# Optimization experiments

Hardware: AMD Instinct MI355X
Metric: run time of the kernel (lower is better)

## Reference

```python
import jax, jax.numpy as jnp
import numpy as np

EMBED_DIM = 1024

def setup_inputs() -> dict:
    key = jax.random.key(0)
    ks = jax.random.split(key, 7)
    D = EMBED_DIM
    x = jax.random.normal(ks[0], (4, 2048, D), dtype=jnp.float32)
    s = 1.0 / np.sqrt(D)
    Wq = jax.random.normal(ks[1], (D, D), dtype=jnp.float32) * s
    bq = jnp.zeros((D,), dtype=jnp.float32)
    Wk = jax.random.normal(ks[2], (D, D), dtype=jnp.float32) * s
    bk = jnp.zeros((D,), dtype=jnp.float32)
    Wv = jax.random.normal(ks[3], (D, D), dtype=jnp.float32) * s
    bv = jnp.zeros((D,), dtype=jnp.float32)
    return {"x": x, "Wq": Wq, "bq": bq, "Wk": Wk, "bk": bk, "Wv": Wv, "bv": bv}

def reference(x, Wq, bq, Wk, bk, Wv, bv):
    # x: [B,S,D]; torch Linear: x @ W.T + b -> here W is stored as [D_in, D_out]
    Q = jnp.einsum('bsd,de->bse', x, Wq) + bq
    K = jnp.einsum('bsd,de->bse', x, Wk) + bk
    V = jnp.einsum('bsd,de->bse', x, Wv) + bv
    scale = 1.0 / jnp.sqrt(jnp.asarray(x.shape[-1], dtype=x.dtype))
    scores = jnp.einsum('bqd,bkd->bqk', Q, K) * scale  # [B,S,S]
    probs = jax.nn.softmax(scores, axis=-1)
    # dropout is identity in eval mode
    return jnp.einsum('bqk,bkd->bqd', probs, V)
```

## Files before the change

### kernel.cpp

```cpp
#include <hip/hip_runtime.h>
#include <hip/hip_bf16.h>
#include <hip/hip_fp16.h>
#include <stdint.h>
#include <stddef.h>
#include <string.h>

#define D_EMB 1024
#define SEQ   2048
#define BATCH 4

typedef short bf16x8  __attribute__((ext_vector_type(8)));
typedef short short8  __attribute__((ext_vector_type(8)));
typedef float f32x4   __attribute__((ext_vector_type(4)));

#define AS1 __attribute__((address_space(1)))
#define AS3 __attribute__((address_space(3)))

static __device__ __forceinline__ void async_copy16(const void* g, void* l) {
  __builtin_amdgcn_global_load_lds((const AS1 void*)g, (AS3 void*)l, 16, 0, 0);
}

static __device__ __forceinline__ void gemm128(
    const __hip_bfloat16* __restrict__ A, int lda,
    const __hip_bfloat16* __restrict__ Bt, int ldb,
    int K, f32x4 (&acc)[4][4])
{
  __shared__ __hip_bfloat16 ldsA[2][128 * 64];
  __shared__ __hip_bfloat16 ldsB[2][128 * 64];

  const int t    = threadIdx.x;
  const int wave = t >> 6;
  const int lane = t & 63;
  const int quad = lane >> 4;
  const int lr   = lane & 15;
  const int wr   = wave >> 1;
  const int wc   = wave & 1;

  const int r0 = t >> 3;
  const int c0 = (((t & 7) ^ (r0 & 7)) * 8);

  const __hip_bfloat16* gA = A  + (size_t)r0 * lda + c0;
  const __hip_bfloat16* gB = Bt + (size_t)r0 * ldb + c0;

  const int niter = K >> 6;

  {
    char* lA = (char*)ldsA[0] + wave * 1024;
    char* lB = (char*)ldsB[0] + wave * 1024;
#pragma unroll
    for (int ch = 0; ch < 4; ch++) {
      async_copy16(gA + (size_t)(32 * ch) * lda, lA + 4096 * ch);
      async_copy16(gB + (size_t)(32 * ch) * ldb, lB + 4096 * ch);
    }
  }

  int buf = 0;
  for (int it = 0; it < niter; ++it) {
    __syncthreads();

    if (it + 1 < niter) {
      const int k0 = (it + 1) << 6;
      char* lA = (char*)ldsA[buf ^ 1] + wave * 1024;
      char* lB = (char*)ldsB[buf ^ 1] + wave * 1024;
#pragma unroll
      for (int ch = 0; ch < 4; ch++) {
        async_copy16(gA + k0 + (size_t)(32 * ch) * lda, lA + 4096 * ch);
        async_copy16(gB + k0 + (size_t)(32 * ch) * ldb, lB + 4096 * ch);
      }
    }

    const __hip_bfloat16* bA = ldsA[buf];
    const __hip_bfloat16* bB = ldsB[buf];
#pragma unroll
    for (int kk = 0; kk < 64; kk += 32) {
      bf16x8 aF[4], bF[4];
      const int lc = (kk >> 3) + quad;
      const int pc = (lc ^ (lr & 7)) * 8;
#pragma unroll
      for (int i = 0; i < 4; i++)
        aF[i] = *(const bf16x8*)&bA[(wr * 64 + i * 16 + lr) * 64 + pc];
#pragma unroll
      for (int j = 0; j < 4; j++)
        bF[j] = *(const bf16x8*)&bB[(wc * 64 + j * 16 + lr) * 64 + pc];

#pragma unroll
      for (int i = 0; i < 4; i++)
#pragma unroll
        for (int j = 0; j < 4; j++)
          acc[i][j] = __builtin_amdgcn_mfma_f32_16x16x32_bf16(aF[i], bF[j], acc[i][j], 0, 0, 0);
    }
    buf ^= 1;
  }
}

#define ZERO_ACC(acc)                         \
  {                                           \
    f32x4 _z = {0.f, 0.f, 0.f, 0.f};          \
    _Pragma("unroll")                         \
    for (int _i = 0; _i < 4; _i++)            \
      _Pragma("unroll")                       \
      for (int _j = 0; _j < 4; _j++)          \
        acc[_i][_j] = _z;                     \
  }

__global__ __launch_bounds__(256) void prep_kernel(
    const float* __restrict__ x,
    const float* __restrict__ Wq,
    const float* __restrict__ Wk,
    const float* __restrict__ Wv,
    __hip_bfloat16* __restrict__ xb,
    __hip_bfloat16* __restrict__ Wt3)
{
  const int tx = threadIdx.x, ty = threadIdx.y;
  if (blockIdx.z == 3) {
    const int tid = ty * 32 + tx;
    const size_t base = ((size_t)blockIdx.y * 32 + blockIdx.x) * 8192;
#pragma unroll
    for (int p = 0; p < 8; p++) {
      const size_t i = base + p * 1024 + tid * 4;
      const float4 v = *(const float4*)(x + i);
      __hip_bfloat16 o[4] = {__float2bfloat16(v.x), __float2bfloat16(v.y),
                             __float2bfloat16(v.z), __float2bfloat16(v.w)};
      *(uint64_t*)(xb + i) = *(uint64_t*)o;
    }
    return;
  }
  const float* src = (blockIdx.z == 0) ? Wq : (blockIdx.z == 1) ? Wk : Wv;
  __hip_bfloat16* dst = Wt3 + (size_t)blockIdx.z * D_EMB * D_EMB;
  __shared__ __hip_bfloat16 tile[32][33];
  const int x0 = blockIdx.x * 32;
  const int y0 = blockIdx.y * 32;
#pragma unroll
  for (int i = 0; i < 32; i += 8)
    tile[ty + i][tx] = __float2bfloat16(src[(size_t)(y0 + ty + i) * D_EMB + (x0 + tx)]);
  __syncthreads();
#pragma unroll
  for (int i = 0; i < 32; i += 8)
    dst[(size_t)(x0 + ty + i) * D_EMB + (y0 + tx)] = tile[tx][ty + i];
}

__global__ __launch_bounds__(256) void qkv_kernel(
    const __hip_bfloat16* __restrict__ xb,
    const __hip_bfloat16* __restrict__ Wt3,
    const float* __restrict__ bq,
    const float* __restrict__ bk,
    const float* __restrict__ bv,
    __hip_bfloat16* __restrict__ Q,
    __hip_bfloat16* __restrict__ Kb,
    __hip_bfloat16* __restrict__ Vt)
{
  const int mat = blockIdx.z;
  const int m0  = blockIdx.x * 128;
  const int n0  = blockIdx.y * 128;

  f32x4 acc[4][4];
  ZERO_ACC(acc);

  gemm128(xb + (size_t)m0 * D_EMB, D_EMB,
          Wt3 + (size_t)mat * D_EMB * D_EMB + (size_t)n0 * D_EMB, D_EMB,
          D_EMB, acc);

  const float* bias = (mat == 0) ? bq : (mat == 1) ? bk : bv;

  const int t = threadIdx.x;
  const int wave = t >> 6, lane = t & 63;
  const int quad = lane >> 4, lr = lane & 15;
  const int wr = wave >> 1, wc = wave & 1;

#pragma unroll
  for (int i = 0; i < 4; i++) {
#pragma unroll
    for (int j = 0; j < 4; j++) {
      const int n = n0 + wc * 64 + j * 16 + lr;
      const float bb = bias[n];
      const int mbase = m0 + wr * 64 + i * 16 + quad * 4;
      if (mat == 2) {
        const int b = mbase >> 11, s = mbase & 2047;
        __hip_bfloat16 pk[4];
#pragma unroll
        for (int r = 0; r < 4; r++) pk[r] = __float2bfloat16(acc[i][j][r] + bb);
        *(uint64_t*)&Vt[(size_t)b * D_EMB * SEQ + (size_t)n * SEQ + s] = *(uint64_t*)pk;
      } else {
        __hip_bfloat16* dst = (mat == 0) ? Q : Kb;
#pragma unroll
        for (int r = 0; r < 4; r++)
          dst[(size_t)(mbase + r) * D_EMB + n] = __float2bfloat16(acc[i][j][r] + bb);
      }
    }
  }
}

__global__ __launch_bounds__(256) void scores_kernel(
    const __hip_bfloat16* __restrict__ Q,
    const __hip_bfloat16* __restrict__ Kb,
    __half* __restrict__ Sc)
{
  const int b  = blockIdx.z;
  const int m0 = blockIdx.y * 128;
  const int n0 = blockIdx.x * 128;

  f32x4 acc[4][4];
  ZERO_ACC(acc);

  gemm128(Q  + (size_t)b * SEQ * D_EMB + (size_t)m0 * D_EMB, D_EMB,
          Kb + (size_t)b * SEQ * D_EMB + (size_t)n0 * D_EMB, D_EMB,
          D_EMB, acc);

  __half* out = Sc + (size_t)b * SEQ * SEQ;
  const float scale = 0.03125f;

  const int t = threadIdx.x;
  const int wave = t >> 6, lane = t & 63;
  const int quad = lane >> 4, lr = lane & 15;
  const int wr = wave >> 1, wc = wave & 1;

#pragma unroll
  for (int i = 0; i < 4; i++)
#pragma unroll
    for (int j = 0; j < 4; j++) {
      const int n = n0 + wc * 64 + j * 16 + lr;
#pragma unroll
      for (int r = 0; r < 4; r++) {
        const int m = m0 + wr * 64 + i * 16 + quad * 4 + r;
        out[(size_t)m * SEQ + n] = __float2half(acc[i][j][r] * scale);
      }
    }
}

__global__ __launch_bounds__(256) void softmax_kernel(
    const __half* __restrict__ Sc, __hip_bfloat16* __restrict__ P)
{
  const int row = blockIdx.x;
  const __half* src = Sc + (size_t)row * SEQ;
  const int t = threadIdx.x;
  const int wave = t >> 6, lane = t & 63;

  const short8 raw = *(const short8*)(src + t * 8);
  float v[8];
#pragma unroll
  for (int i = 0; i < 8; i++) {
    const short si = raw[i];
    __half h;
    memcpy(&h, &si, sizeof(h));
    v[i] = __half2float(h);
  }

  float m = v[0];
#pragma unroll
  for (int i = 1; i < 8; i++) m = fmaxf(m, v[i]);
#pragma unroll
  for (int o = 32; o > 0; o >>= 1) m = fmaxf(m, __shfl_xor(m, o));

  __shared__ float redm[4];
  __shared__ float reds[4];
  if (lane == 0) redm[wave] = m;
  __syncthreads();
  m = fmaxf(fmaxf(redm[0], redm[1]), fmaxf(redm[2], redm[3]));

  float e[8], s = 0.f;
#pragma unroll
  for (int i = 0; i < 8; i++) { e[i] = __expf(v[i] - m); s += e[i]; }
#pragma unroll
  for (int o = 32; o > 0; o >>= 1) s += __shfl_xor(s, o);
  if (lane == 0) reds[wave] = s;
  __syncthreads();
  s = reds[0] + reds[1] + reds[2] + reds[3];

  const float inv = 1.f / s;
  short8 outp;
#pragma unroll
  for (int i = 0; i < 8; i++) {
    const __hip_bfloat16 b = __float2bfloat16(e[i] * inv);
    short sb;
    memcpy(&sb, &b, sizeof(sb));
    outp[i] = sb;
  }
  *(short8*)(P + (size_t)row * SEQ + t * 8) = outp;
}

__global__ __launch_bounds__(256) void pv_kernel(
    const __hip_bfloat16* __restrict__ P,
    const __hip_bfloat16* __restrict__ Vt,
    float* __restrict__ out)
{
  const int b  = blockIdx.z;
  const int m0 = blockIdx.y * 128;
  const int n0 = blockIdx.x * 128;

  f32x4 acc[4][4];
  ZERO_ACC(acc);

  gemm128(P  + (size_t)b * SEQ * SEQ   + (size_t)m0 * SEQ, SEQ,
          Vt + (size_t)b * D_EMB * SEQ + (size_t)n0 * SEQ, SEQ,
          SEQ, acc);

  float* o = out + (size_t)b * SEQ * D_EMB;

  const int t = threadIdx.x;
  const int wave = t >> 6, lane = t & 63;
  const int quad = lane >> 4, lr = lane & 15;
  const int wr = wave >> 1, wc = wave & 1;

#pragma unroll
  for (int i = 0; i < 4; i++)
#pragma unroll
    for (int j = 0; j < 4; j++) {
      const int n = n0 + wc * 64 + j * 16 + lr;
#pragma unroll
      for (int r = 0; r < 4; r++) {
        const int m = m0 + wr * 64 + i * 16 + quad * 4 + r;
        o[(size_t)m * D_EMB + n] = acc[i][j][r];
      }
    }
}

extern "C" void kernel_launch(void* const* d_in, const int* in_sizes, int n_in,
                              void* d_out, int out_size, void* d_ws, size_t ws_size,
                              hipStream_t stream) {
  const float* x  = (const float*)d_in[0];
  const float* Wq = (const float*)d_in[1];
  const float* bq = (const float*)d_in[2];
  const float* Wk = (const float*)d_in[3];
  const float* bk = (const float*)d_in[4];
  const float* Wv = (const float*)d_in[5];
  const float* bv = (const float*)d_in[6];
  float* out = (float*)d_out;

  char* ws = (char*)d_ws;
  __hip_bfloat16* xb  = (__hip_bfloat16*)(ws);
  __hip_bfloat16* Wt3 = (__hip_bfloat16*)(ws + 16777216);
  __hip_bfloat16* Q   = (__hip_bfloat16*)(ws + 23068672);
  __hip_bfloat16* Kb  = (__hip_bfloat16*)(ws + 39845888);
  __hip_bfloat16* Vt  = (__hip_bfloat16*)(ws + 56623104);
  __half*         Sc  = (__half*)        (ws + 73400320);
  __hip_bfloat16* P   = (__hip_bfloat16*)(ws + 140509184);

  prep_kernel  <<<dim3(32, 32, 4), dim3(32, 8), 0, stream>>>(x, Wq, Wk, Wv, xb, Wt3);
  qkv_kernel   <<<dim3(64, 8, 3),  256,        0, stream>>>(xb, Wt3, bq, bk, bv, Q, Kb, Vt);
  scores_kernel<<<dim3(16, 16, 4), 256,        0, stream>>>(Q, Kb, Sc);
  softmax_kernel<<<dim3(8192),     256,        0, stream>>>(Sc, P);
  pv_kernel    <<<dim3(8, 16, 4),  256,        0, stream>>>(P, Vt, out);
}
```

Measured before the change: 265.4 us.

## Replace 128x128 GEMM tile with 256x256 8-wave ping-pong pipelined GEMM

Replaces the shared 128x128 double-buffered GEMM with a 256x256 tile computed by 512 threads (8 waves). Global-to-LDS staging is interleaved in half-tile chunks with MFMA quarters, using explicit vmcnt waits, barriers and s_setprio to overlap loads with compute. The larger tile raises operand reuse and cuts global traffic, and all three GEMM kernels (qkv, scores, pv) switch to the new grid and launch sizes. The cost is double the LDS and accumulator registers per block plus many barriers, and far fewer blocks, for example 128 for pv and 256 for scores on a 256-CU part, which may leave the GPU underfilled.

```diff
diff --git a/kernel.cpp b/kernel.cpp
--- a/kernel.cpp
+++ b/kernel.cpp
@@ -20,76 +20,162 @@
   __builtin_amdgcn_global_load_lds((const AS1 void*)g, (AS3 void*)l, 16, 0, 0);
 }
 
-static __device__ __forceinline__ void gemm128(
+
+#define BAR     __builtin_amdgcn_s_barrier()
+#define VMCNT4  asm volatile("s_waitcnt vmcnt(4)" ::: "memory")
+#define VMCNT0  asm volatile("s_waitcnt vmcnt(0)" ::: "memory")
+
+#define STAGE_A(buf, h, kt) do {                                              \
+    const __hip_bfloat16* _g = gA + (size_t)((h) * 128) * lda + ((kt) << 6);  \
+    char* _l = (char*)sA + (buf) * 32768 + (h) * 16384 + wave * 1024;         \
+    async_copy16(_g, _l);                                                     \
+    async_copy16(_g + (size_t)64 * lda, _l + 8192);                           \
+  } while (0)
+#define STAGE_B(buf, h, kt) do {                                              \
+    const __hip_bfloat16* _g = gB + (size_t)((h) * 128) * ldb + ((kt) << 6);  \
+    char* _l = (char*)sB + (buf) * 32768 + (h) * 16384 + wave * 1024;         \
+    async_copy16(_g, _l);                                                     \
+    async_copy16(_g + (size_t)64 * ldb, _l + 8192);                           \
+  } while (0)
+
+#define LOAD_A(aF, lbuf, h) do {                                              \
+    const __hip_bfloat16* _b = (lbuf) + (wr * 128 + (h) * 64 + lr) * 64;      \
+    _Pragma("unroll")                                                         \
+    for (int _i = 0; _i < 4; _i++) {                                          \
+      aF[_i][0] = *(const bf16x8*)&_b[_i * 1024 + pc0];                       \
+      aF[_i][1] = *(const bf16x8*)&_b[_i * 1024 + pc1];                       \
+    }                                                                         \
+  } while (0)
+#define LOAD_B(bF, lbuf, g) do {                                              \
+    const __hip_bfloat16* _b = (lbuf) + (wc * 64 + (g) * 32 + lr) * 64;       \
+    _Pragma("unroll")                                                         \
+    for (int _j = 0; _j < 2; _j++) {                                          \
+      bF[_j][0] = *(const bf16x8*)&_b[_j * 1024 + pc0];                       \
+      bF[_j][1] = *(const bf16x8*)&_b[_j * 1024 + pc1];                       \
+    }                                                                         \
+  } while (0)
+
+#define MFMA_Q(aF, bF, h, g) do {                                             \
+    __builtin_amdgcn_s_setprio(1);                                            \
+    _Pragma("unroll")                                                         \
+    for (int _i = 0; _i < 4; _i++)                                            \
+      _Pragma("unroll")                                                       \
+      for (int _j = 0; _j < 2; _j++) {                                        \
+        acc[(h) * 4 + _i][(g) * 2 + _j] =                                     \
+          __builtin_amdgcn_mfma_f32_16x16x32_bf16(aF[_i][0], bF[_j][0],       \
+              acc[(h) * 4 + _i][(g) * 2 + _j], 0, 0, 0);                      \
+        acc[(h) * 4 + _i][(g) * 2 + _j] =                                     \
+          __builtin_amdgcn_mfma_f32_16x16x32_bf16(aF[_i][1], bF[_j][1],       \
+              acc[(h) * 4 + _i][(g) * 2 + _j], 0, 0, 0);                      \
+      }                                                                       \
+    __builtin_amdgcn_s_setprio(0);                                            \
+  } while (0)
+
+static __device__ __forceinline__ void gemm256(
     const __hip_bfloat16* __restrict__ A, int lda,
     const __hip_bfloat16* __restrict__ Bt, int ldb,
-    int K, f32x4 (&acc)[4][4])
-{
-  __shared__ __hip_bfloat16 ldsA[2][128 * 64];
-  __shared__ __hip_bfloat16 ldsB[2][128 * 64];
+    int K, f32x4 (&acc)[8][4])
+{
+  __shared__ __hip_bfloat16 sA[2][128 * 64 * 2];
+  __shared__ __hip_bfloat16 sB[2][128 * 64 * 2];
 
   const int t    = threadIdx.x;
   const int wave = t >> 6;
   const int lane = t & 63;
   const int quad = lane >> 4;
   const int lr   = lane & 15;
-  const int wr   = wave >> 1;
-  const int wc   = wave & 1;
+  const int wr   = wave >> 2;
+  const int wc   = wave & 3;
 
   const int r0 = t >> 3;
-  const int c0 = (((t & 7) ^ (r0 & 7)) * 8);
-
-  const __hip_bfloat16* gA = A  + (size_t)r0 * lda + c0;
-  const __hip_bfloat16* gB = Bt + (size_t)r0 * ldb + c0;
-
-  const int niter = K >> 6;
+  const int cs = (((t & 7) ^ (r0 & 7)) << 3);
+  const __hip_bfloat16* gA = A  + (size_t)r0 * lda + cs;
+  const __hip_bfloat16* gB = Bt + (size_t)r0 * ldb + cs;
+
+  const int pc0 = ((quad)     ^ (lr & 7)) << 3;
+  const int pc1 = ((quad + 4) ^ (lr & 7)) << 3;
+
+  const __hip_bfloat16* const lA0 = sA[0];
+  const __hip_bfloat16* const lA1 = sA[1];
+  const __hip_bfloat16* const lB0 = sB[0];
+  const __hip_bfloat16* const lB1 = sB[1];
+
+  const int nt    = K >> 6;
+  const int niter = nt >> 1;
+
+  STAGE_A(0, 0, 0);
+  STAGE_A(0, 1, 0);
+  STAGE_B(0, 0, 0);
+  STAGE_B(0, 1, 0);
+  STAGE_A(1, 0, 1);
+  STAGE_B(1, 1, 1);
+  VMCNT4;
+  BAR;
+
+  bf16x8 aF[4][2], bFa[2][2], bFb[2][2];
+
+  for (int j = 0; j < niter - 1; ++j) {
+    const int tb = 2 * j + 1, tc = tb + 1, td = tb + 2;
+
+    LOAD_A(aF, lA0, 0); LOAD_B(bFa, lB0, 0);
+    STAGE_B(1, 0, tb);
+    BAR; MFMA_Q(aF, bFa, 0, 0); BAR;
+
+    LOAD_B(bFb, lB0, 1);
+    STAGE_A(1, 1, tb);
+    BAR; MFMA_Q(aF, bFb, 0, 1); BAR;
+
+    LOAD_A(aF, lA0, 1);
+    STAGE_A(0, 0, tc);
+    BAR; MFMA_Q(aF, bFb, 1, 1); BAR;
+
+    STAGE_B(0, 1, tc);
+    VMCNT4;
+    BAR; MFMA_Q(aF, bFa, 1, 0); BAR;
+
+    LOAD_A(aF, lA1, 0); LOAD_B(bFa, lB1, 0);
+    STAGE_B(0, 0, tc);
+    BAR; MFMA_Q(aF, bFa, 0, 0); BAR;
+
+    LOAD_B(bFb, lB1, 1);
+    STAGE_A(0, 1, tc);
+    BAR; MFMA_Q(aF, bFb, 0, 1); BAR;
+
+    LOAD_A(aF, lA1, 1);
+    STAGE_A(1, 0, td);
+    BAR; MFMA_Q(aF, bFb, 1, 1); BAR;
+
+    STAGE_B(1, 1, td);
+    VMCNT4;
+    BAR; MFMA_Q(aF, bFa, 1, 0); BAR;
+  }
 
   {
-    char* lA = (char*)ldsA[0] + wave * 1024;
-    char* lB = (char*)ldsB[0] + wave * 1024;
-#pragma unroll
-    for (int ch = 0; ch < 4; ch++) {
-      async_copy16(gA + (size_t)(32 * ch) * lda, lA + 4096 * ch);
-      async_copy16(gB + (size_t)(32 * ch) * ldb, lB + 4096 * ch);
-    }
-  }
-
-  int buf = 0;
-  for (int it = 0; it < niter; ++it) {
-    __syncthreads();
-
-    if (it + 1 < niter) {
-      const int k0 = (it + 1) << 6;
-      char* lA = (char*)ldsA[buf ^ 1] + wave * 1024;
-      char* lB = (char*)ldsB[buf ^ 1] + wave * 1024;
-#pragma unroll
-      for (int ch = 0; ch < 4; ch++) {
-        async_copy16(gA + k0 + (size_t)(32 * ch) * lda, lA + 4096 * ch);
-        async_copy16(gB + k0 + (size_t)(32 * ch) * ldb, lB + 4096 * ch);
-      }
-    }
-
-    const __hip_bfloat16* bA = ldsA[buf];
-    const __hip_bfloat16* bB = ldsB[buf];
-#pragma unroll
-    for (int kk = 0; kk < 64; kk += 32) {
-      bf16x8 aF[4], bF[4];
-      const int lc = (kk >> 3) + quad;
-      const int pc = (lc ^ (lr & 7)) * 8;
-#pragma unroll
-      for (int i = 0; i < 4; i++)
-        aF[i] = *(const bf16x8*)&bA[(wr * 64 + i * 16 + lr) * 64 + pc];
-#pragma unroll
-      for (int j = 0; j < 4; j++)
-        bF[j] = *(const bf16x8*)&bB[(wc * 64 + j * 16 + lr) * 64 + pc];
-
-#pragma unroll
-      for (int i = 0; i < 4; i++)
-#pragma unroll
-        for (int j = 0; j < 4; j++)
-          acc[i][j] = __builtin_amdgcn_mfma_f32_16x16x32_bf16(aF[i], bF[j], acc[i][j], 0, 0, 0);
-    }
-    buf ^= 1;
+    const int tb = nt - 1;
+    LOAD_A(aF, lA0, 0); LOAD_B(bFa, lB0, 0);
+    STAGE_B(1, 0, tb);
+    BAR; MFMA_Q(aF, bFa, 0, 0); BAR;
+
+    LOAD_B(bFb, lB0, 1);
+    STAGE_A(1, 1, tb);
+    BAR; MFMA_Q(aF, bFb, 0, 1); BAR;
+
+    LOAD_A(aF, lA0, 1);
+    BAR; MFMA_Q(aF, bFb, 1, 1); BAR;
+
+    VMCNT0;
+    BAR; MFMA_Q(aF, bFa, 1, 0); BAR;
+
+    LOAD_A(aF, lA1, 0); LOAD_B(bFa, lB1, 0);
+    BAR; MFMA_Q(aF, bFa, 0, 0); BAR;
+
+    LOAD_B(bFb, lB1, 1);
+    BAR; MFMA_Q(aF, bFb, 0, 1); BAR;
+
+    LOAD_A(aF, lA1, 1);
+    BAR; MFMA_Q(aF, bFb, 1, 1); BAR;
+
+    MFMA_Q(aF, bFa, 1, 0);
   }
 }
 
@@ -97,7 +183,7 @@
   {                                           \
     f32x4 _z = {0.f, 0.f, 0.f, 0.f};          \
     _Pragma("unroll")                         \
-    for (int _i = 0; _i < 4; _i++)            \
+    for (int _i = 0; _i < 8; _i++)            \
       _Pragma("unroll")                       \
       for (int _j = 0; _j < 4; _j++)          \
         acc[_i][_j] = _z;                     \
@@ -139,7 +225,7 @@
     dst[(size_t)(x0 + ty + i) * D_EMB + (y0 + tx)] = tile[tx][ty + i];
 }
 
-__global__ __launch_bounds__(256) void qkv_kernel(
+__global__ __launch_bounds__(512, 2) void qkv_kernel(
     const __hip_bfloat16* __restrict__ xb,
     const __hip_bfloat16* __restrict__ Wt3,
     const float* __restrict__ bq,
@@ -150,13 +236,13 @@
     __hip_bfloat16* __restrict__ Vt)
 {
   const int mat = blockIdx.z;
-  const int m0  = blockIdx.x * 128;
-  const int n0  = blockIdx.y * 128;
-
-  f32x4 acc[4][4];
+  const int m0  = blockIdx.x * 256;
+  const int n0  = blockIdx.y * 256;
+
+  f32x4 acc[8][4];
   ZERO_ACC(acc);
 
-  gemm128(xb + (size_t)m0 * D_EMB, D_EMB,
+  gemm256(xb + (size_t)m0 * D_EMB, D_EMB,
           Wt3 + (size_t)mat * D_EMB * D_EMB + (size_t)n0 * D_EMB, D_EMB,
           D_EMB, acc);
 
@@ -165,15 +251,15 @@
   const int t = threadIdx.x;
   const int wave = t >> 6, lane = t & 63;
   const int quad = lane >> 4, lr = lane & 15;
-  const int wr = wave >> 1, wc = wave & 1;
-
-#pragma unroll
-  for (int i = 0; i < 4; i++) {
+  const int wr = wave >> 2, wc = wave & 3;
+
+#pragma unroll
+  for (int i = 0; i < 8; i++) {
 #pragma unroll
     for (int j = 0; j < 4; j++) {
       const int n = n0 + wc * 64 + j * 16 + lr;
       const float bb = bias[n];
-      const int mbase = m0 + wr * 64 + i * 16 + quad * 4;
+      const int mbase = m0 + wr * 128 + i * 16 + quad * 4;
       if (mat == 2) {
         const int b = mbase >> 11, s = mbase & 2047;
         __hip_bfloat16 pk[4];
@@ -190,19 +276,19 @@
   }
 }
 
-__global__ __launch_bounds__(256) void scores_kernel(
+__global__ __launch_bounds__(512, 2) void scores_kernel(
     const __hip_bfloat16* __restrict__ Q,
     const __hip_bfloat16* __restrict__ Kb,
     __half* __restrict__ Sc)
 {
   const int b  = blockIdx.z;
-  const int m0 = blockIdx.y * 128;
-  const int n0 = blockIdx.x * 128;
-
-  f32x4 acc[4][4];
+  const int m0 = blockIdx.y * 256;
+  const int n0 = blockIdx.x * 256;
+
+  f32x4 acc[8][4];
   ZERO_ACC(acc);
 
-  gemm128(Q  + (size_t)b * SEQ * D_EMB + (size_t)m0 * D_EMB, D_EMB,
+  gemm256(Q  + (size_t)b * SEQ * D_EMB + (size_t)m0 * D_EMB, D_EMB,
           Kb + (size_t)b * SEQ * D_EMB + (size_t)n0 * D_EMB, D_EMB,
           D_EMB, acc);
 
@@ -212,16 +298,16 @@
   const int t = threadIdx.x;
   const int wave = t >> 6, lane = t & 63;
   const int quad = lane >> 4, lr = lane & 15;
-  const int wr = wave >> 1, wc = wave & 1;
-
-#pragma unroll
-  for (int i = 0; i < 4; i++)
+  const int wr = wave >> 2, wc = wave & 3;
+
+#pragma unroll
+  for (int i = 0; i < 8; i++)
 #pragma unroll
     for (int j = 0; j < 4; j++) {
       const int n = n0 + wc * 64 + j * 16 + lr;
 #pragma unroll
       for (int r = 0; r < 4; r++) {
-        const int m = m0 + wr * 64 + i * 16 + quad * 4 + r;
+        const int m = m0 + wr * 128 + i * 16 + quad * 4 + r;
         out[(size_t)m * SEQ + n] = __float2half(acc[i][j][r] * scale);
       }
     }
@@ -278,19 +364,19 @@
   *(short8*)(P + (size_t)row * SEQ + t * 8) = outp;
 }
 
-__global__ __launch_bounds__(256) void pv_kernel(
+__global__ __launch_bounds__(512, 2) void pv_kernel(
     const __hip_bfloat16* __restrict__ P,
     const __hip_bfloat16* __restrict__ Vt,
     float* __restrict__ out)
 {
   const int b  = blockIdx.z;
-  const int m0 = blockIdx.y * 128;
-  const int n0 = blockIdx.x * 128;
-
-  f32x4 acc[4][4];
+  const int m0 = blockIdx.y * 256;
+  const int n0 = blockIdx.x * 256;
+
+  f32x4 acc[8][4];
   ZERO_ACC(acc);
 
-  gemm128(P  + (size_t)b * SEQ * SEQ   + (size_t)m0 * SEQ, SEQ,
+  gemm256(P  + (size_t)b * SEQ * SEQ   + (size_t)m0 * SEQ, SEQ,
           Vt + (size_t)b * D_EMB * SEQ + (size_t)n0 * SEQ, SEQ,
           SEQ, acc);
 
@@ -299,16 +385,16 @@
   const int t = threadIdx.x;
   const int wave = t >> 6, lane = t & 63;
   const int quad = lane >> 4, lr = lane & 15;
-  const int wr = wave >> 1, wc = wave & 1;
-
-#pragma unroll
-  for (int i = 0; i < 4; i++)
+  const int wr = wave >> 2, wc = wave & 3;
+
+#pragma unroll
+  for (int i = 0; i < 8; i++)
 #pragma unroll
     for (int j = 0; j < 4; j++) {
       const int n = n0 + wc * 64 + j * 16 + lr;
 #pragma unroll
       for (int r = 0; r < 4; r++) {
-        const int m = m0 + wr * 64 + i * 16 + quad * 4 + r;
+        const int m = m0 + wr * 128 + i * 16 + quad * 4 + r;
         o[(size_t)m * D_EMB + n] = acc[i][j][r];
       }
     }
@@ -336,8 +422,8 @@
   __hip_bfloat16* P   = (__hip_bfloat16*)(ws + 140509184);
 
   prep_kernel  <<<dim3(32, 32, 4), dim3(32, 8), 0, stream>>>(x, Wq, Wk, Wv, xb, Wt3);
-  qkv_kernel   <<<dim3(64, 8, 3),  256,        0, stream>>>(xb, Wt3, bq, bk, bv, Q, Kb, Vt);
-  scores_kernel<<<dim3(16, 16, 4), 256,        0, stream>>>(Q, Kb, Sc);
+  qkv_kernel   <<<dim3(32, 4, 3),  512,        0, stream>>>(xb, Wt3, bq, bk, bv, Q, Kb, Vt);
+  scores_kernel<<<dim3(8, 8, 4),   512,        0, stream>>>(Q, Kb, Sc);
   softmax_kernel<<<dim3(8192),     256,        0, stream>>>(Sc, P);
-  pv_kernel    <<<dim3(8, 16, 4),  256,        0, stream>>>(P, Vt, out);
-}
+  pv_kernel    <<<dim3(4, 8, 4),   512,        0, stream>>>(P, Vt, out);
+}
```

Result: slower. 270.9 us (+2.1%).
